# Kernel tuning notes

Hardware: AMD Instinct MI355X
Metric: run time of the kernel (lower is better)

The kernel has to match this reference:

```python
import jax, jax.numpy as jnp
import numpy as np

N = 100000       # nodes
DEG = 16         # fixed out/in degree used to build CSR
E = N * DEG      # edges
D_IN = 128       # in_feats
D_OUT = 256      # out_feats
K = 32           # maxk k_value


def _xavier_uniform(key, shape, gain):
    fan_out, fan_in = shape
    bound = gain * np.sqrt(6.0 / (fan_in + fan_out))
    return jax.random.uniform(key, shape, jnp.float32, -bound, bound)


def setup_inputs() -> dict:
    key = jax.random.key(0)
    ks = jax.random.split(key, 6)
    feat = jax.random.normal(ks[0], (N, D_IN), jnp.float32)
    topk_values = jax.random.uniform(ks[1], (N, K), jnp.float32)
    topk_indices = jax.random.randint(ks[2], (N, K), 0, D_IN).astype(jnp.int32)
    # CSR graph: fixed degree -> indptr is arange*DEG; random destinations
    indptr = (jnp.arange(N + 1) * DEG).astype(jnp.int32)
    indices = jax.random.randint(ks[3], (E,), 0, N).astype(jnp.int32)
    # set_graph_data: csr weight[e] = 1 / clamp(in_degree(dst), 1)
    in_deg = jax.ops.segment_sum(jnp.ones(E, jnp.float32), indices, num_segments=N)
    in_deg = jnp.maximum(in_deg, 1.0)
    csr_values = 1.0 / in_deg[indices]
    gain = np.sqrt(2.0)  # calculate_gain('relu')
    w_neigh = _xavier_uniform(ks[4], (D_OUT, D_IN), gain)
    w_self = _xavier_uniform(ks[5], (D_OUT, D_IN), gain)
    b_self = jnp.zeros((D_OUT,), jnp.float32)
    return {"feat": feat, "topk_values": topk_values, "csr_values": csr_values,
            "w_neigh": w_neigh, "w_self": w_self, "b_self": b_self,
            "topk_indices": topk_indices, "indptr": indptr, "indices": indices}


def reference(feat, topk_values, csr_values, w_neigh, w_self, b_self,
              topk_indices, indptr, indices):
    # Densify the k-sparse MaxK features: x[n, topk_indices[n, j]] = topk_values[n, j]
    x = jnp.zeros((N, D_IN), feat.dtype).at[
        jnp.arange(N)[:, None], topk_indices].add(topk_values)
    # Edge-weight-normalized SpMM over CSR: out[row] += w[e] * x[col[e]]
    row_ids = jnp.repeat(jnp.arange(N), jnp.diff(indptr), total_repeat_length=E)
    msgs = x[indices] * csr_values[:, None]          # [E, D_IN]
    agg = jax.ops.segment_sum(msgs, row_ids, num_segments=N)  # [N, D_IN]
    # lin_before_mp is False (in_feats <= out_feats): project after aggregation
    h_neigh = agg @ w_neigh.T                        # [N, D_OUT]
    rst = feat @ w_self.T + b_self + h_neigh         # fc_self(h_self) + h_neigh
    return rst
```

## Files before the change

kernel.cpp:

```cpp
#include <hip/hip_runtime.h>
#include <hip/hip_bf16.h>
#include <stdint.h>

#define N_NODES 100000
#define DEG 16
#define D_IN 128
#define D_OUT 256
#define K_TOP 32
#define K_CAT 256

typedef __attribute__((ext_vector_type(8))) short short8;
typedef __attribute__((ext_vector_type(4))) float floatx4;

__device__ __forceinline__ unsigned pack_bf16_rne(float f) {
    union { float f; unsigned u; } c; c.f = f;
    unsigned u = c.u;
    return (u + 0x7fffu + ((u >> 16) & 1u)) >> 16;
}
__device__ __forceinline__ float bf16lo_to_f(unsigned lo16) {
    union { unsigned u; float f; } c; c.u = lo16 << 16; return c.f;
}

typedef __attribute__((address_space(1))) void as1_void;
typedef __attribute__((address_space(3))) void as3_void;
__device__ __forceinline__ void gload_lds16(const void* g, void* l) {
    __builtin_amdgcn_global_load_lds((as1_void*)g, (as3_void*)l, 16, 0, 0);
}

__global__ __launch_bounds__(256) void k_packw(const float* __restrict__ w_self,
                                               const float* __restrict__ w_neigh,
                                               unsigned short* __restrict__ bmat) {
    int o = blockIdx.x;
    int k = threadIdx.x;
    float v = (k < D_IN) ? w_self[o * D_IN + k] : w_neigh[o * D_IN + (k - D_IN)];
    bmat[o * K_CAT + k] = (unsigned short)pack_bf16_rne(v);
}

#define DROWS 64
__global__ __launch_bounds__(256) void k_densify(const float* __restrict__ topk_v,
                                                 const int* __restrict__ topk_i,
                                                 const float* __restrict__ feat,
                                                 unsigned short* __restrict__ xbf,
                                                 unsigned short* __restrict__ fbf) {
    __shared__ float sx[DROWS * D_IN];
    const int t = threadIdx.x;
    const int row0 = blockIdx.x * DROWS;

    #pragma unroll
    for (int p = 0; p < 8; ++p)
        *(floatx4*)&sx[(t + p * 256) * 4] = (floatx4){0.f, 0.f, 0.f, 0.f};
    __syncthreads();

    const size_t tbase = (size_t)row0 * K_TOP;
    #pragma unroll
    for (int p = 0; p < 8; ++p) {
        int q = t + p * 256;
        int r = q >> 5;
        if (row0 + r < N_NODES) {
            int   ci = topk_i[tbase + q];
            float cv = topk_v[tbase + q];
            atomicAdd(&sx[r * D_IN + ci], cv);
        }
    }
    __syncthreads();

    #pragma unroll
    for (int p = 0; p < 16; ++p) {
        int d = t + p * 256;
        int r = d >> 6;
        int c2 = (d & 63) * 2;
        if (row0 + r < N_NODES) {
            float2 v = *(const float2*)&sx[r * D_IN + c2];
            ((unsigned*)(xbf + (size_t)(row0 + r) * D_IN))[d & 63] =
                pack_bf16_rne(v.x) | (pack_bf16_rne(v.y) << 16);
        }
    }

    #pragma unroll
    for (int p = 0; p < 8; ++p) {
        int q = t + p * 256;
        int r = q >> 5;
        int c4 = (q & 31) * 4;
        if (row0 + r < N_NODES) {
            float4 f = *(const float4*)(feat + (size_t)(row0 + r) * D_IN + c4);
            uint2 pk;
            pk.x = pack_bf16_rne(f.x) | (pack_bf16_rne(f.y) << 16);
            pk.y = pack_bf16_rne(f.z) | (pack_bf16_rne(f.w) << 16);
            ((uint2*)(fbf + (size_t)(row0 + r) * D_IN))[q & 31] = pk;
        }
    }
}

#define BM 128
#define BN 256
#define BK 32
#define NTA 4
#define NT  8

__global__ __launch_bounds__(512, 2) void k_fused(const float* __restrict__ csr_w,
                                                  const int* __restrict__ col_idx,
                                                  const unsigned short* __restrict__ xbf,
                                                  const unsigned short* __restrict__ fbf,
                                                  const unsigned short* __restrict__ bmat,
                                                  const float* __restrict__ bias,
                                                  float* __restrict__ out) {
    __shared__ __align__(16) unsigned short Agg[BM * 128];
    __shared__ __align__(16) unsigned short As[2][BM * BK];
    __shared__ __align__(16) unsigned short Bs[2][BN * BK];
    const int t    = threadIdx.x;
    const int lane = t & 63, wave = t >> 6;
    const int l16  = lane & 15, quad = lane >> 4;
    const int row0 = blockIdx.x * BM;

    const int a_r = wave * 16 + (lane >> 2);
    const int a_c = (lane & 3) * 8;
    int a_gr = row0 + a_r; if (a_gr >= N_NODES) a_gr = N_NODES - 1;
    const unsigned short* gA  = fbf  + (size_t)a_gr * D_IN + a_c;
    const unsigned short* gB0 = bmat + (size_t)a_r        * K_CAT + a_c;
    const unsigned short* gB1 = bmat + (size_t)(a_r + 128) * K_CAT + a_c;

#define STAGE_A(buf, tt) gload_lds16(gA + (tt) * BK, &As[buf][wave * 16 * BK])
#define STAGE_B(buf, tt) do {                                                 \
        gload_lds16(gB0 + (tt) * BK, &Bs[buf][(wave * 16)       * BK]);       \
        gload_lds16(gB1 + (tt) * BK, &Bs[buf][(wave * 16 + 128) * BK]);       \
    } while (0)

    STAGE_A(0, 0);
    STAGE_B(0, 0);

    const int ql = lane & 15, qb = lane & 48;
    const int qrow = wave * 4 + (lane >> 4);

    int cc[4]; float ww[4];
    #pragma unroll
    for (int p = 0; p < 4; ++p) {
        const int gr = row0 + p * 32 + qrow;
        cc[p] = 0; ww[p] = 0.f;
        if (gr < N_NODES) {
            cc[p] = __builtin_nontemporal_load(col_idx + (size_t)gr * DEG + ql);
            ww[p] = __builtin_nontemporal_load(csr_w   + (size_t)gr * DEG + ql);
        }
    }

    uint4 vva[8], vvb[8];
    #pragma unroll
    for (int e = 0; e < 8; ++e) {
        int col = __shfl(cc[0], qb | e);
        vva[e] = *(const uint4*)(xbf + (size_t)col * D_IN + ql * 8);
    }
    float a[8] = {0.f, 0.f, 0.f, 0.f, 0.f, 0.f, 0.f, 0.f};

    #pragma unroll
    for (int s = 0; s < 8; ++s) {
        const int p  = s >> 1;
        const int e0 = (s & 1) * 8;
        if (s < 7) {
            const int np  = (s + 1) >> 1;
            const int ne0 = ((s + 1) & 1) * 8;
            #pragma unroll
            for (int e = 0; e < 8; ++e) {
                int col = __shfl(cc[np], qb | (ne0 + e));
                if (s & 1) vva[e] = *(const uint4*)(xbf + (size_t)col * D_IN + ql * 8);
                else       vvb[e] = *(const uint4*)(xbf + (size_t)col * D_IN + ql * 8);
            }
        }
        #pragma unroll
        for (int e = 0; e < 8; ++e) {
            float we = __shfl(ww[p], qb | (e0 + e));
            uint4 v = (s & 1) ? vvb[e] : vva[e];
            a[0] += we * bf16lo_to_f(v.x & 0xffffu);
            a[1] += we * bf16lo_to_f(v.x >> 16);
            a[2] += we * bf16lo_to_f(v.y & 0xffffu);
            a[3] += we * bf16lo_to_f(v.y >> 16);
            a[4] += we * bf16lo_to_f(v.z & 0xffffu);
            a[5] += we * bf16lo_to_f(v.z >> 16);
            a[6] += we * bf16lo_to_f(v.w & 0xffffu);
            a[7] += we * bf16lo_to_f(v.w >> 16);
        }
        if (s & 1) {
            const int r = p * 32 + qrow;
            uint4 pk;
            pk.x = pack_bf16_rne(a[0]) | (pack_bf16_rne(a[1]) << 16);
            pk.y = pack_bf16_rne(a[2]) | (pack_bf16_rne(a[3]) << 16);
            pk.z = pack_bf16_rne(a[4]) | (pack_bf16_rne(a[5]) << 16);
            pk.w = pack_bf16_rne(a[6]) | (pack_bf16_rne(a[7]) << 16);
            *(uint4*)&Agg[r * 128 + ((ql * 8) ^ ((r & 7) << 3))] = pk;
            #pragma unroll
            for (int z = 0; z < 8; ++z) a[z] = 0.f;
        }
    }

    const int wr = wave >> 2, wc = wave & 3;
    floatx4 acc[4][4];
    #pragma unroll
    for (int i = 0; i < 4; ++i)
        #pragma unroll
        for (int j = 0; j < 4; ++j)
            acc[i][j] = (floatx4){0.f, 0.f, 0.f, 0.f};

    __syncthreads();

    #pragma unroll
    for (int tt = 0; tt < NT; ++tt) {
        const int cur = tt & 1;
        if (tt + 1 < NTA) STAGE_A(cur ^ 1, tt + 1);
        if (tt + 1 < NT)  STAGE_B(cur ^ 1, tt + 1);

        short8 afr[4], bfr[4];
        if (tt < NTA) {
            #pragma unroll
            for (int i = 0; i < 4; ++i)
                afr[i] = *(const short8*)&As[cur][(wr * 64 + i * 16 + l16) * BK + quad * 8];
        } else {
            const int c0 = (tt - NTA) * 32 + quad * 8;
            #pragma unroll
            for (int i = 0; i < 4; ++i) {
                const int m = wr * 64 + i * 16 + l16;
                afr[i] = *(const short8*)&Agg[m * 128 + (c0 ^ ((m & 7) << 3))];
            }
        }
        #pragma unroll
        for (int j = 0; j < 4; ++j)
            bfr[j] = *(const short8*)&Bs[cur][(wc * 64 + j * 16 + l16) * BK + quad * 8];

        #pragma unroll
        for (int i = 0; i < 4; ++i)
            #pragma unroll
            for (int j = 0; j < 4; ++j)
                acc[i][j] = __builtin_amdgcn_mfma_f32_16x16x32_bf16(bfr[j], afr[i], acc[i][j], 0, 0, 0);

        if (tt + 1 < NT) __syncthreads();
    }

    #pragma unroll
    for (int j = 0; j < 4; ++j) {
        const int cg = wc * 64 + j * 16 + quad * 4;
        const floatx4 bv = *(const floatx4*)&bias[cg];
        #pragma unroll
        for (int i = 0; i < 4; ++i) {
            const int gr = row0 + wr * 64 + i * 16 + l16;
            if (gr < N_NODES) {
                floatx4 v = acc[i][j] + bv;
                __builtin_nontemporal_store(v, (floatx4*)(out + (size_t)gr * D_OUT + cg));
            }
        }
    }
#undef STAGE_A
#undef STAGE_B
}

extern "C" void kernel_launch(void* const* d_in, const int* in_sizes, int n_in,
                              void* d_out, int out_size, void* d_ws, size_t ws_size,
                              hipStream_t stream) {
    const float* feat    = (const float*)d_in[0];
    const float* topk_v  = (const float*)d_in[1];
    const float* csr_w   = (const float*)d_in[2];
    const float* w_neigh = (const float*)d_in[3];
    const float* w_self  = (const float*)d_in[4];
    const float* b_self  = (const float*)d_in[5];
    const int*   topk_i  = (const int*)d_in[6];
    const int*   indices = (const int*)d_in[8];
    float* out = (float*)d_out;

    unsigned short* xbf  = (unsigned short*)d_ws;
    unsigned short* fbf  = xbf + (size_t)N_NODES * D_IN;
    unsigned short* bmat = fbf + (size_t)N_NODES * D_IN;

    k_packw<<<dim3(256), dim3(256), 0, stream>>>(w_self, w_neigh, bmat);
    k_densify<<<dim3((N_NODES + DROWS - 1) / DROWS), dim3(256), 0, stream>>>(topk_v, topk_i, feat, xbf, fbf);
    k_fused<<<dim3((N_NODES + BM - 1) / BM), dim3(512), 0, stream>>>(
        csr_w, indices, xbf, fbf, bmat, b_self, out);
}
```

Measured before the change: 271.1 us.

## Merge weight packing into densify kernel and read B fragments from global

Folds the weight-packing kernel into the densify kernel as extra blocks, removing one launch. In the fused GEMM, B fragments are now loaded straight from global memory (L2/L1-resident bmat) into registers instead of being staged through double-buffered LDS. This cuts LDS usage and most of the barriers in the K loop. The cost is higher global/L1 load latency on each MFMA step, with no prefetch to hide it.

```diff
diff --git a/kernel.cpp b/kernel.cpp
--- a/kernel.cpp
+++ b/kernel.cpp
@@ -27,23 +27,24 @@
     __builtin_amdgcn_global_load_lds((as1_void*)g, (as3_void*)l, 16, 0, 0);
 }
 
-__global__ __launch_bounds__(256) void k_packw(const float* __restrict__ w_self,
-                                               const float* __restrict__ w_neigh,
-                                               unsigned short* __restrict__ bmat) {
-    int o = blockIdx.x;
-    int k = threadIdx.x;
-    float v = (k < D_IN) ? w_self[o * D_IN + k] : w_neigh[o * D_IN + (k - D_IN)];
-    bmat[o * K_CAT + k] = (unsigned short)pack_bf16_rne(v);
-}
-
+#define DB 1563
 #define DROWS 64
-__global__ __launch_bounds__(256) void k_densify(const float* __restrict__ topk_v,
-                                                 const int* __restrict__ topk_i,
-                                                 const float* __restrict__ feat,
-                                                 unsigned short* __restrict__ xbf,
-                                                 unsigned short* __restrict__ fbf) {
+__global__ __launch_bounds__(256) void k_prep(const float* __restrict__ topk_v,
+                                              const int* __restrict__ topk_i,
+                                              const float* __restrict__ feat,
+                                              const float* __restrict__ w_self,
+                                              const float* __restrict__ w_neigh,
+                                              unsigned short* __restrict__ xbf,
+                                              unsigned short* __restrict__ fbf,
+                                              unsigned short* __restrict__ bmat) {
     __shared__ float sx[DROWS * D_IN];
     const int t = threadIdx.x;
+    if (blockIdx.x >= DB) {
+        const int o = blockIdx.x - DB;
+        float v = (t < D_IN) ? w_self[o * D_IN + t] : w_neigh[o * D_IN + (t - D_IN)];
+        bmat[o * K_CAT + t] = (unsigned short)pack_bf16_rne(v);
+        return;
+    }
     const int row0 = blockIdx.x * DROWS;
 
     #pragma unroll
@@ -106,7 +107,6 @@
                                                   float* __restrict__ out) {
     __shared__ __align__(16) unsigned short Agg[BM * 128];
     __shared__ __align__(16) unsigned short As[2][BM * BK];
-    __shared__ __align__(16) unsigned short Bs[2][BN * BK];
     const int t    = threadIdx.x;
     const int lane = t & 63, wave = t >> 6;
     const int l16  = lane & 15, quad = lane >> 4;
@@ -115,18 +115,11 @@
     const int a_r = wave * 16 + (lane >> 2);
     const int a_c = (lane & 3) * 8;
     int a_gr = row0 + a_r; if (a_gr >= N_NODES) a_gr = N_NODES - 1;
-    const unsigned short* gA  = fbf  + (size_t)a_gr * D_IN + a_c;
-    const unsigned short* gB0 = bmat + (size_t)a_r        * K_CAT + a_c;
-    const unsigned short* gB1 = bmat + (size_t)(a_r + 128) * K_CAT + a_c;
+    const unsigned short* gA = fbf + (size_t)a_gr * D_IN + a_c;
 
 #define STAGE_A(buf, tt) gload_lds16(gA + (tt) * BK, &As[buf][wave * 16 * BK])
-#define STAGE_B(buf, tt) do {                                                 \
-        gload_lds16(gB0 + (tt) * BK, &Bs[buf][(wave * 16)       * BK]);       \
-        gload_lds16(gB1 + (tt) * BK, &Bs[buf][(wave * 16 + 128) * BK]);       \
-    } while (0)
 
     STAGE_A(0, 0);
-    STAGE_B(0, 0);
 
     const int ql = lane & 15, qb = lane & 48;
     const int qrow = wave * 4 + (lane >> 4);
@@ -191,6 +184,7 @@
     }
 
     const int wr = wave >> 2, wc = wave & 3;
+    const unsigned short* gBw = bmat + (size_t)(wc * 64 + l16) * K_CAT + quad * 8;
     floatx4 acc[4][4];
     #pragma unroll
     for (int i = 0; i < 4; ++i)
@@ -204,9 +198,11 @@
     for (int tt = 0; tt < NT; ++tt) {
         const int cur = tt & 1;
         if (tt + 1 < NTA) STAGE_A(cur ^ 1, tt + 1);
-        if (tt + 1 < NT)  STAGE_B(cur ^ 1, tt + 1);
 
         short8 afr[4], bfr[4];
+        #pragma unroll
+        for (int j = 0; j < 4; ++j)
+            bfr[j] = *(const short8*)(gBw + (size_t)j * 16 * K_CAT + tt * BK);
         if (tt < NTA) {
             #pragma unroll
             for (int i = 0; i < 4; ++i)
@@ -219,9 +215,6 @@
                 afr[i] = *(const short8*)&Agg[m * 128 + (c0 ^ ((m & 7) << 3))];
             }
         }
-        #pragma unroll
-        for (int j = 0; j < 4; ++j)
-            bfr[j] = *(const short8*)&Bs[cur][(wc * 64 + j * 16 + l16) * BK + quad * 8];
 
         #pragma unroll
         for (int i = 0; i < 4; ++i)
@@ -229,7 +222,7 @@
             for (int j = 0; j < 4; ++j)
                 acc[i][j] = __builtin_amdgcn_mfma_f32_16x16x32_bf16(bfr[j], afr[i], acc[i][j], 0, 0, 0);
 
-        if (tt + 1 < NT) __syncthreads();
+        if (tt + 1 < NTA) __syncthreads();
     }
 
     #pragma unroll
@@ -246,7 +239,6 @@
         }
     }
 #undef STAGE_A
-#undef STAGE_B
 }
 
 extern "C" void kernel_launch(void* const* d_in, const int* in_sizes, int n_in,
@@ -266,8 +258,8 @@
     unsigned short* fbf  = xbf + (size_t)N_NODES * D_IN;
     unsigned short* bmat = fbf + (size_t)N_NODES * D_IN;
 
-    k_packw<<<dim3(256), dim3(256), 0, stream>>>(w_self, w_neigh, bmat);
-    k_densify<<<dim3((N_NODES + DROWS - 1) / DROWS), dim3(256), 0, stream>>>(topk_v, topk_i, feat, xbf, fbf);
+    k_prep<<<dim3(DB + 256), dim3(256), 0, stream>>>(
+        topk_v, topk_i, feat, w_self, w_neigh, xbf, fbf, bmat);
     k_fused<<<dim3((N_NODES + BM - 1) / BM), dim3(512), 0, stream>>>(
         csr_w, indices, xbf, fbf, bmat, b_self, out);
 }
```

Result: slower. 292.9 us (+8.0%).
